# Kernel tuning notes

Hardware: AMD Instinct MI355X
Metric: run time of the kernel (lower is better)

Reference implementation:

```python
import jax, jax.numpy as jnp
import numpy as np

N_NODES = 100000
N_EDGES = 1600000
N_OBS = 48
HIDDEN = 48
N_ACT = 32


def setup_inputs() -> dict:
    key = jax.random.key(0)
    ks = jax.random.split(key, 6)
    x = jax.random.normal(ks[0], (N_OBS, N_NODES), dtype=jnp.float32)
    onehot = jax.random.uniform(ks[1], (1, N_NODES), dtype=jnp.float32)
    W1 = jax.random.normal(ks[2], (N_OBS, HIDDEN), dtype=jnp.float32) * (1.0 / np.sqrt(N_OBS))
    b1 = jnp.zeros((HIDDEN,), dtype=jnp.float32)
    W2 = jax.random.normal(ks[3], (HIDDEN, N_ACT), dtype=jnp.float32) * (1.0 / np.sqrt(HIDDEN))
    b2 = jnp.zeros((N_ACT,), dtype=jnp.float32)
    edge_index = jax.random.randint(ks[4], (2, N_EDGES), 0, N_NODES, dtype=jnp.int64)
    return {"x": x, "onehot": onehot, "W1": W1, "b1": b1, "W2": W2, "b2": b2, "edge_index": edge_index}


def reference(x, onehot, W1, b1, W2, b2, edge_index):
    # graph.x is stored transposed; forward does x = graph.x.T -> [N, F]
    h = x.T  # [N, n_obs]
    n = h.shape[0]
    # GCNConv default: add self-loops, symmetric deg^-1/2 normalization
    loops = jnp.arange(n, dtype=edge_index.dtype)
    row = jnp.concatenate([edge_index[0], loops])  # source nodes
    col = jnp.concatenate([edge_index[1], loops])  # target nodes
    deg = jax.ops.segment_sum(jnp.ones(row.shape, dtype=h.dtype), col, num_segments=n)
    dinv = jnp.where(deg > 0, jax.lax.rsqrt(jnp.maximum(deg, 1.0)), 0.0)
    norm = dinv[row] * dinv[col]  # [E+N]

    def conv(feat, W, b):
        feat = feat @ W                         # tiny dense GEMM [N, d_out]
        msg = norm[:, None] * feat[row]         # gather + scale  [E+N, d_out]
        return jax.ops.segment_sum(msg, col, num_segments=n) + b  # scatter-add

    # dropout is identity in eval mode
    h = jax.nn.relu(conv(h, W1, b1))
    h = conv(h, W2, b2)                          # [N, n_actions]
    return onehot @ h                            # [1, n_actions]
```

## Files before the change

kernel.cpp:

```cpp
#include <hip/hip_runtime.h>

#define CAP 64
#define NBUCK 512
#define NPB 196
#define NPH 98
#define GCAPH 1792
#define LCAP 24
#define GCAP 3584
#define NBIN 256
#define QAMAX0 6.0f
#define QS0 (127.0f / QAMAX0)
#define QAMAX1 4.0f
#define INVQS1 (QAMAX1 / 127.0f)
#define SMEM1 53248

__device__ __forceinline__ void bin_pass(const int* __restrict__ pay,
                                         const int* __restrict__ key, int E,
                                         int* __restrict__ bcur,
                                         unsigned* __restrict__ barr,
                                         char* smem, int binBlk) {
    unsigned* buf = (unsigned*)smem;
    int* cnt  = (int*)(buf + NBUCK * LCAP);
    int* base = cnt + NBUCK;
    for (int i = threadIdx.x; i < NBUCK; i += 256) cnt[i] = 0;
    __syncthreads();
    int epb = (E + NBIN - 1) / NBIN;
    int start = binBlk * epb;
    int end = min(E, start + epb);
    for (int e0 = start + threadIdx.x; e0 < end; e0 += 256 * 4) {
        int rr[4], cc[4];
#pragma unroll
        for (int k = 0; k < 4; k++) {
            int e = e0 + k * 256;
            if (e < end) { rr[k] = pay[e]; cc[k] = key[e]; }
        }
#pragma unroll
        for (int k = 0; k < 4; k++) {
            int e = e0 + k * 256;
            if (e < end) {
                int b = cc[k] / NPB;
                unsigned ent = ((unsigned)rr[k] << 8) | (unsigned)(cc[k] - b * NPB);
                int p = atomicAdd(&cnt[b], 1);
                if (p < LCAP) buf[b * LCAP + p] = ent;
                else {
                    int gp = atomicAdd(&bcur[b], 1);
                    if (gp < GCAP) barr[(size_t)b * GCAP + gp] = ent;
                }
            }
        }
    }
    __syncthreads();
    for (int b = threadIdx.x; b < NBUCK; b += 256)
        base[b] = atomicAdd(&bcur[b], min(cnt[b], LCAP));
    __syncthreads();
    for (int idx = threadIdx.x; idx < NBUCK * LCAP; idx += 256) {
        int b = idx / LCAP, slot = idx - b * LCAP;
        if (slot < min(cnt[b], LCAP)) {
            int gp = base[b] + slot;
            if (gp < GCAP) barr[(size_t)b * GCAP + gp] = buf[idx];
        }
    }
}

__launch_bounds__(256)
__global__ void k_bin_gemm(const int* __restrict__ row, const int* __restrict__ col,
                           int E, int* __restrict__ bcur1, unsigned* __restrict__ barr1,
                           int* __restrict__ bcur2, unsigned* __restrict__ barr2,
                           const float* __restrict__ x, const float* __restrict__ W1,
                           const float* __restrict__ onehot,
                           unsigned* __restrict__ q0, float* __restrict__ ohsum,
                           float* __restrict__ out, int N) {
    __shared__ __align__(16) char smem[SMEM1];
    if (blockIdx.x < NBIN) {
        bin_pass(row, col, E, bcur1, barr1, smem, blockIdx.x);
    } else if (blockIdx.x < 2 * NBIN) {
        bin_pass(col, row, E, bcur2, barr2, smem, blockIdx.x - NBIN);
    } else {
        if (blockIdx.x == 2 * NBIN && threadIdx.x < 32) out[threadIdx.x] = 0.f;
        float* Ws = (float*)smem;
        float* ohred = Ws + 48 * 48;
        for (int i = threadIdx.x; i < 48 * 48; i += 256) Ws[i] = W1[i];
        __syncthreads();
        int n = (blockIdx.x - 2 * NBIN) * 256 + threadIdx.x;
        float oh = 0.f;
        if (n < N) {
            float acc[48];
#pragma unroll
            for (int j = 0; j < 48; j++) acc[j] = 0.f;
            for (int k = 0; k < 48; k++) {
                float xv = x[(size_t)k * N + n];
#pragma unroll
                for (int j = 0; j < 48; j++) acc[j] += xv * Ws[k * 48 + j];
            }
            oh = onehot[n];
            unsigned* qp = q0 + (size_t)n * 12;
#pragma unroll
            for (int p = 0; p < 12; p++) {
                unsigned u = 0;
#pragma unroll
                for (int k = 0; k < 4; k++) {
                    int b = __float2int_rn(acc[4 * p + k] * QS0);
                    b = (b < -127 ? -127 : (b > 127 ? 127 : b)) + 128;
                    u |= ((unsigned)b) << (8 * k);
                }
                qp[p] = u;
            }
        }
        ohred[threadIdx.x] = oh;
        __syncthreads();
        for (int off = 128; off > 0; off >>= 1) {
            if (threadIdx.x < off) ohred[threadIdx.x] += ohred[threadIdx.x + off];
            __syncthreads();
        }
        if (threadIdx.x == 0) atomicAdd(ohsum, ohred[0]);
    }
}

__launch_bounds__(256)
__global__ void k_build(const unsigned* __restrict__ barr1,
                        const int* __restrict__ bcur1,
                        int* __restrict__ csr, long long* __restrict__ sd,
                        const float* __restrict__ onehot, float* __restrict__ t,
                        const unsigned* __restrict__ q0, unsigned* __restrict__ q,
                        int N) {
    __shared__ int csr_s[GCAPH];
    __shared__ int cnt_s[NPH];
    __shared__ int scan_s[128];
    __shared__ int cur_s[NPH];
    int b = blockIdx.x >> 1, half = blockIdx.x & 1;
    int lnbase = half * NPH;
    for (int i = threadIdx.x; i < NPH; i += 256) cnt_s[i] = 0;
    __syncthreads();
    int bn = min(bcur1[b], GCAP);
    const unsigned* bp = barr1 + (size_t)b * GCAP;
    int nbase = b * NPB + lnbase;
    for (int i = threadIdx.x; i < bn; i += 256) {
        int lnh = (int)(bp[i] & 0xffu) - lnbase;
        if ((unsigned)lnh < NPH) atomicAdd(&cnt_s[lnh], 1);
    }
    __syncthreads();
    int v = (threadIdx.x < NPH) ? cnt_s[threadIdx.x] : 0;
    if (threadIdx.x < 128) scan_s[threadIdx.x] = v;
    __syncthreads();
    for (int off = 1; off < 128; off <<= 1) {
        int tv = (threadIdx.x >= off && threadIdx.x < 128) ? scan_s[threadIdx.x - off] : 0;
        __syncthreads();
        if (threadIdx.x < 128) scan_s[threadIdx.x] += tv;
        __syncthreads();
    }
    if (threadIdx.x < NPH) cur_s[threadIdx.x] = scan_s[threadIdx.x] - v;
    __syncthreads();
    for (int i = threadIdx.x; i < bn; i += 256) {
        unsigned e = bp[i];
        int lnh = (int)(e & 0xffu) - lnbase;
        if ((unsigned)lnh < NPH) {
            int p = atomicAdd(&cur_s[lnh], 1);
            if (p < GCAPH) csr_s[p] = (int)(e >> 8);
        }
    }
    __syncthreads();
    int tot = min(scan_s[NPH - 1], GCAPH);
    int gbase = b * GCAP + half * GCAPH;
    for (int i = threadIdx.x; i < tot; i += 256)
        csr[gbase + i] = csr_s[i];
    for (int i = threadIdx.x; i < NPH; i += 256) {
        int n = nbase + i;
        if (n < N) {
            int d = cnt_s[i];
            long long st = (long long)(gbase + (scan_s[i] - d));
            sd[n] = st | ((long long)d << 32);
            t[n] = onehot[n] * rsqrtf((float)(d + 1));
        }
    }
    for (int idx = threadIdx.x; idx < NPH * 12; idx += 256) {
        int i = idx / 12, p = idx - i * 12;
        int n = nbase + i;
        if (n < N) {
            float r = 1.5f * rsqrtf((float)(cnt_s[i] + 1));
            unsigned u = q0[(size_t)n * 12 + p];
            unsigned o = 0;
#pragma unroll
            for (int k = 0; k < 4; k++) {
                int bq = (int)((u >> (8 * k)) & 0xffu) - 128;
                int nb = __float2int_rn((float)bq * r);
                nb = (nb < -127 ? -127 : (nb > 127 ? 127 : nb)) + 128;
                o |= ((unsigned)nb) << (8 * k);
            }
            q[(size_t)n * 12 + p] = o;
        }
    }
}

__launch_bounds__(256)
__global__ void k_gather_buildw(const unsigned* __restrict__ barr2,
                                const int* __restrict__ bcur2,
                                const float* __restrict__ t, float* __restrict__ w,
                                const int* __restrict__ csr,
                                const long long* __restrict__ sd,
                                const unsigned* __restrict__ q,
                                const float* __restrict__ b1, const float* __restrict__ W2,
                                float* __restrict__ g2, int N) {
    __shared__ float W2s[48 * 32];
    __shared__ float a1s[16][48];
    const unsigned M = 0x00FF00FFu;
    if (blockIdx.x < NBUCK) {
        float* wacc = (float*)W2s;
        int b = blockIdx.x;
        for (int i = threadIdx.x; i < NPB; i += 256) wacc[i] = 0.f;
        __syncthreads();
        int bn = min(bcur2[b], GCAP);
        const unsigned* bp = barr2 + (size_t)b * GCAP;
        int nbase = b * NPB;
        for (int i = threadIdx.x; i < bn; i += 256) {
            unsigned e = __builtin_nontemporal_load(&bp[i]);
            atomicAdd(&wacc[e & 0xffu], t[e >> 8]);
        }
        __syncthreads();
        for (int i = threadIdx.x; i < NPB; i += 256) {
            int n = nbase + i;
            if (n < N) w[n] = wacc[i] + t[n];
        }
        return;
    }
    for (int i = threadIdx.x; i < 48 * 32; i += 256) W2s[i] = W2[i];
    int wv = threadIdx.x >> 6, lane = threadIdx.x & 63;
    int quarter = lane >> 4, lane16 = lane & 15;
    int s = lane16 >> 2, j = lane16 & 3;
    int node = wv * 4 + quarter;
    int c = (blockIdx.x - NBUCK) * 16 + node;
    float dv = 0.f;
    if (c < N) {
        long long sdv = __builtin_nontemporal_load(&sd[c]);
        int beg = (int)(sdv & 0xffffffffLL), dg = (int)(sdv >> 32);
        int dd = dg < CAP ? dg : CAP;
        dv = rsqrtf((float)(dg + 1));
        int idx[4];
#pragma unroll
        for (int k = 0; k < 4; k++)
            idx[k] = (16 * k + lane16 < dd)
                         ? __builtin_nontemporal_load(&csr[beg + 16 * k + lane16]) : 0;
        unsigned ux[16], uy[16], uz[16];
#pragma unroll
        for (int g = 0; g < 16; g++) {
            if (4 * g < dd) {
                int e = 4 * g + s;
                int src = __shfl(idx[g >> 2], quarter * 16 + (e & 15));
                bool vld = (e < dd);
                const unsigned* qp = q + (size_t)src * 12 + 3 * j;
                ux[g] = vld ? qp[0] : 0u;
                uy[g] = vld ? qp[1] : 0u;
                uz[g] = vld ? qp[2] : 0u;
            }
        }
        unsigned aE0 = 0, aO0 = 0, aE1 = 0, aO1 = 0, aE2 = 0, aO2 = 0;
        if (s == 0) {
            const unsigned* qp = q + (size_t)c * 12 + 3 * j;
            unsigned x0 = qp[0], x1 = qp[1], x2 = qp[2];
            aE0 = x0 & M; aO0 = (x0 >> 8) & M;
            aE1 = x1 & M; aO1 = (x1 >> 8) & M;
            aE2 = x2 & M; aO2 = (x2 >> 8) & M;
        }
#pragma unroll
        for (int g = 0; g < 16; g++) {
            if (4 * g < dd) {
                aE0 += ux[g] & M; aO0 += (ux[g] >> 8) & M;
                aE1 += uy[g] & M; aO1 += (uy[g] >> 8) & M;
                aE2 += uz[g] & M; aO2 += (uz[g] >> 8) & M;
            }
        }
#pragma unroll
        for (int off = 8; off >= 4; off >>= 1) {
            aE0 += (unsigned)__shfl_down((int)aE0, off, 16);
            aO0 += (unsigned)__shfl_down((int)aO0, off, 16);
            aE1 += (unsigned)__shfl_down((int)aE1, off, 16);
            aO1 += (unsigned)__shfl_down((int)aO1, off, 16);
            aE2 += (unsigned)__shfl_down((int)aE2, off, 16);
            aO2 += (unsigned)__shfl_down((int)aO2, off, 16);
        }
        if (s == 0) {
            float cnt = (float)(dd + 1);
            float gsc = dv * INVQS1;
            float corr = 128.f * cnt;
            float S0 = (float)(aE0 & 0xffffu), S2 = (float)(aE0 >> 16);
            float S1 = (float)(aO0 & 0xffffu), S3 = (float)(aO0 >> 16);
            float S4 = (float)(aE1 & 0xffffu), S6 = (float)(aE1 >> 16);
            float S5 = (float)(aO1 & 0xffffu), S7 = (float)(aO1 >> 16);
            float S8 = (float)(aE2 & 0xffffu), S10 = (float)(aE2 >> 16);
            float S9 = (float)(aO2 & 0xffffu), S11 = (float)(aO2 >> 16);
            const float4* b4 = (const float4*)b1;
            float4 ba = b4[3 * j], bb = b4[3 * j + 1], bc = b4[3 * j + 2];
            float4 oa, ob, oc;
            oa.x = fmaxf(gsc * (S0 - corr) + ba.x, 0.f);
            oa.y = fmaxf(gsc * (S1 - corr) + ba.y, 0.f);
            oa.z = fmaxf(gsc * (S2 - corr) + ba.z, 0.f);
            oa.w = fmaxf(gsc * (S3 - corr) + ba.w, 0.f);
            ob.x = fmaxf(gsc * (S4 - corr) + bb.x, 0.f);
            ob.y = fmaxf(gsc * (S5 - corr) + bb.y, 0.f);
            ob.z = fmaxf(gsc * (S6 - corr) + bb.z, 0.f);
            ob.w = fmaxf(gsc * (S7 - corr) + bb.w, 0.f);
            oc.x = fmaxf(gsc * (S8 - corr) + bc.x, 0.f);
            oc.y = fmaxf(gsc * (S9 - corr) + bc.y, 0.f);
            oc.z = fmaxf(gsc * (S10 - corr) + bc.z, 0.f);
            oc.w = fmaxf(gsc * (S11 - corr) + bc.w, 0.f);
            float4* as4 = (float4*)a1s[node];
            as4[3 * j] = oa; as4[3 * j + 1] = ob; as4[3 * j + 2] = oc;
        }
    }
    __syncthreads();
    if (c < N) {
        int f0 = lane16 * 2;
        float a = 0.f, b = 0.f;
#pragma unroll
        for (int k = 0; k < 48; k++) {
            float av = a1s[node][k];
            a += av * W2s[k * 32 + f0];
            b += av * W2s[k * 32 + f0 + 1];
        }
        __builtin_nontemporal_store(dv * a, &g2[(size_t)c * 32 + f0]);
        __builtin_nontemporal_store(dv * b, &g2[(size_t)c * 32 + f0 + 1]);
    }
}

__global__ void k_final3(const float* __restrict__ g2, const float* __restrict__ w,
                         const float* __restrict__ ohsum, const float* __restrict__ b2,
                         float* __restrict__ out, int N) {
    __shared__ float s[256];
    int tid = threadIdx.x;
    int total = N * 32;
    int stride = gridDim.x * 256;
    float acc = 0.f;
    for (int i = blockIdx.x * 256 + tid; i < total; i += stride)
        acc += w[i >> 5] * g2[i];
    s[tid] = acc;
    __syncthreads();
    for (int off = 128; off >= 32; off >>= 1) {
        if (tid < off) s[tid] += s[tid + off];
        __syncthreads();
    }
    if (tid < 32) {
        float v = s[tid];
        if (blockIdx.x == 0) v += b2[tid] * ohsum[0];
        atomicAdd(&out[tid], v);
    }
}

extern "C" void kernel_launch(void* const* d_in, const int* in_sizes, int n_in,
                              void* d_out, int out_size, void* d_ws, size_t ws_size,
                              hipStream_t stream) {
    const float* x      = (const float*)d_in[0];
    const float* onehot = (const float*)d_in[1];
    const float* W1     = (const float*)d_in[2];
    const float* b1     = (const float*)d_in[3];
    const float* W2     = (const float*)d_in[4];
    const float* b2     = (const float*)d_in[5];
    const int*   ei     = (const int*)d_in[6];

    int N = in_sizes[1];
    int E = in_sizes[6] / 2;
    const int* row = ei;
    const int* col = ei + E;

    char* wsb = (char*)d_ws;
    int*       bcur1  = (int*)wsb;          wsb += 512 * 4;
    int*       bcur2  = (int*)wsb;          wsb += 512 * 4;
    float*     ohsum  = (float*)wsb;        wsb += 2 * 4;
    unsigned*  barr1  = (unsigned*)wsb;     wsb += (size_t)NBUCK * GCAP * 4;
    unsigned*  barr2  = (unsigned*)wsb;     wsb += (size_t)NBUCK * GCAP * 4;
    int*       csr    = (int*)wsb;          wsb += (size_t)NBUCK * GCAP * 4;
    long long* sd     = (long long*)wsb;    wsb += (size_t)N * 8;
    float*     t      = (float*)wsb;        wsb += (size_t)N * 4;
    float*     w      = (float*)wsb;        wsb += (size_t)N * 4;
    unsigned*  q0     = (unsigned*)wsb;     wsb += (size_t)N * 12 * 4;
    unsigned*  q      = (unsigned*)wsb;     wsb += (size_t)N * 12 * 4;
    float*     g2     = (float*)wsb;        wsb += (size_t)N * 32 * 4;

    hipMemsetAsync(bcur1, 0, (512 + 512 + 2) * 4, stream);

    int nGB = (N + 255) / 256;
    int NB = (N + 15) / 16;
    k_bin_gemm<<<2 * NBIN + nGB, 256, 0, stream>>>(row, col, E, bcur1, barr1,
                                                   bcur2, barr2, x, W1, onehot,
                                                   q0, ohsum, (float*)d_out, N);
    k_build<<<2 * NBUCK, 256, 0, stream>>>(barr1, bcur1, csr, sd,
                                           onehot, t, q0, q, N);
    k_gather_buildw<<<NBUCK + NB, 256, 0, stream>>>(barr2, bcur2, t, w,
                                                    csr, sd, q,
                                                    b1, W2, g2, N);
    k_final3<<<256, 256, 0, stream>>>(g2, w, ohsum, b2, (float*)d_out, N);
}
```

Baseline: 205.4 us.

## Replace CSR build with bucket-local shared-memory atomic aggregation of quantized features

```diff
diff --git a/kernel.cpp b/kernel.cpp
--- a/kernel.cpp
+++ b/kernel.cpp
@@ -1,10 +1,9 @@
 #include <hip/hip_runtime.h>
 
-#define CAP 64
 #define NBUCK 512
 #define NPB 196
 #define NPH 98
-#define GCAPH 1792
+#define ACCW 25
 #define LCAP 24
 #define GCAP 3584
 #define NBIN 256
@@ -117,62 +116,31 @@
 }
 
 __launch_bounds__(256)
-__global__ void k_build(const unsigned* __restrict__ barr1,
-                        const int* __restrict__ bcur1,
-                        int* __restrict__ csr, long long* __restrict__ sd,
-                        const float* __restrict__ onehot, float* __restrict__ t,
-                        const unsigned* __restrict__ q0, unsigned* __restrict__ q,
-                        int N) {
-    __shared__ int csr_s[GCAPH];
-    __shared__ int cnt_s[NPH];
-    __shared__ int scan_s[128];
-    __shared__ int cur_s[NPH];
-    int b = blockIdx.x >> 1, half = blockIdx.x & 1;
-    int lnbase = half * NPH;
-    for (int i = threadIdx.x; i < NPH; i += 256) cnt_s[i] = 0;
+__global__ void k_deg_rescale(const unsigned* __restrict__ barr1,
+                              const int* __restrict__ bcur1,
+                              const float* __restrict__ onehot,
+                              int* __restrict__ deg, float* __restrict__ t,
+                              const unsigned* __restrict__ q0,
+                              unsigned* __restrict__ q, int N) {
+    __shared__ int cnt_s[NPB];
+    int b = blockIdx.x;
+    for (int i = threadIdx.x; i < NPB; i += 256) cnt_s[i] = 0;
     __syncthreads();
     int bn = min(bcur1[b], GCAP);
     const unsigned* bp = barr1 + (size_t)b * GCAP;
-    int nbase = b * NPB + lnbase;
-    for (int i = threadIdx.x; i < bn; i += 256) {
-        int lnh = (int)(bp[i] & 0xffu) - lnbase;
-        if ((unsigned)lnh < NPH) atomicAdd(&cnt_s[lnh], 1);
-    }
-    __syncthreads();
-    int v = (threadIdx.x < NPH) ? cnt_s[threadIdx.x] : 0;
-    if (threadIdx.x < 128) scan_s[threadIdx.x] = v;
-    __syncthreads();
-    for (int off = 1; off < 128; off <<= 1) {
-        int tv = (threadIdx.x >= off && threadIdx.x < 128) ? scan_s[threadIdx.x - off] : 0;
-        __syncthreads();
-        if (threadIdx.x < 128) scan_s[threadIdx.x] += tv;
-        __syncthreads();
-    }
-    if (threadIdx.x < NPH) cur_s[threadIdx.x] = scan_s[threadIdx.x] - v;
-    __syncthreads();
-    for (int i = threadIdx.x; i < bn; i += 256) {
-        unsigned e = bp[i];
-        int lnh = (int)(e & 0xffu) - lnbase;
-        if ((unsigned)lnh < NPH) {
-            int p = atomicAdd(&cur_s[lnh], 1);
-            if (p < GCAPH) csr_s[p] = (int)(e >> 8);
-        }
-    }
-    __syncthreads();
-    int tot = min(scan_s[NPH - 1], GCAPH);
-    int gbase = b * GCAP + half * GCAPH;
-    for (int i = threadIdx.x; i < tot; i += 256)
-        csr[gbase + i] = csr_s[i];
-    for (int i = threadIdx.x; i < NPH; i += 256) {
+    for (int i = threadIdx.x; i < bn; i += 256)
+        atomicAdd(&cnt_s[bp[i] & 0xffu], 1);
+    __syncthreads();
+    int nbase = b * NPB;
+    for (int i = threadIdx.x; i < NPB; i += 256) {
         int n = nbase + i;
         if (n < N) {
             int d = cnt_s[i];
-            long long st = (long long)(gbase + (scan_s[i] - d));
-            sd[n] = st | ((long long)d << 32);
+            deg[n] = d;
             t[n] = onehot[n] * rsqrtf((float)(d + 1));
         }
     }
-    for (int idx = threadIdx.x; idx < NPH * 12; idx += 256) {
+    for (int idx = threadIdx.x; idx < NPB * 12; idx += 256) {
         int i = idx / 12, p = idx - i * 12;
         int n = nbase + i;
         if (n < N) {
@@ -186,138 +154,121 @@
                 nb = (nb < -127 ? -127 : (nb > 127 ? 127 : nb)) + 128;
                 o |= ((unsigned)nb) << (8 * k);
             }
-            q[(size_t)n * 12 + p] = o;
+            q[((size_t)n << 4) + p] = o;
         }
     }
 }
 
 __launch_bounds__(256)
-__global__ void k_gather_buildw(const unsigned* __restrict__ barr2,
+__global__ void k_gather_buildw(const unsigned* __restrict__ barr1,
+                                const int* __restrict__ bcur1,
+                                const unsigned* __restrict__ barr2,
                                 const int* __restrict__ bcur2,
+                                const int* __restrict__ deg,
                                 const float* __restrict__ t, float* __restrict__ w,
-                                const int* __restrict__ csr,
-                                const long long* __restrict__ sd,
                                 const unsigned* __restrict__ q,
-                                const float* __restrict__ b1, const float* __restrict__ W2,
+                                const float* __restrict__ b1,
+                                const float* __restrict__ W2,
                                 float* __restrict__ g2, int N) {
+    __shared__ unsigned acc_s[NPH][ACCW];
     __shared__ float W2s[48 * 32];
     __shared__ float a1s[16][48];
+    __shared__ float b1s[48];
+    __shared__ int deg_s[NPH];
     const unsigned M = 0x00FF00FFu;
-    if (blockIdx.x < NBUCK) {
+    int tid = threadIdx.x;
+    if (blockIdx.x >= 2 * NBUCK) {
         float* wacc = (float*)W2s;
-        int b = blockIdx.x;
-        for (int i = threadIdx.x; i < NPB; i += 256) wacc[i] = 0.f;
+        int b = blockIdx.x - 2 * NBUCK;
+        for (int i = tid; i < NPB; i += 256) wacc[i] = 0.f;
         __syncthreads();
         int bn = min(bcur2[b], GCAP);
         const unsigned* bp = barr2 + (size_t)b * GCAP;
         int nbase = b * NPB;
-        for (int i = threadIdx.x; i < bn; i += 256) {
+        for (int i = tid; i < bn; i += 256) {
             unsigned e = __builtin_nontemporal_load(&bp[i]);
             atomicAdd(&wacc[e & 0xffu], t[e >> 8]);
         }
         __syncthreads();
-        for (int i = threadIdx.x; i < NPB; i += 256) {
+        for (int i = tid; i < NPB; i += 256) {
             int n = nbase + i;
             if (n < N) w[n] = wacc[i] + t[n];
         }
         return;
     }
-    for (int i = threadIdx.x; i < 48 * 32; i += 256) W2s[i] = W2[i];
-    int wv = threadIdx.x >> 6, lane = threadIdx.x & 63;
-    int quarter = lane >> 4, lane16 = lane & 15;
-    int s = lane16 >> 2, j = lane16 & 3;
-    int node = wv * 4 + quarter;
-    int c = (blockIdx.x - NBUCK) * 16 + node;
-    float dv = 0.f;
-    if (c < N) {
-        long long sdv = __builtin_nontemporal_load(&sd[c]);
-        int beg = (int)(sdv & 0xffffffffLL), dg = (int)(sdv >> 32);
-        int dd = dg < CAP ? dg : CAP;
-        dv = rsqrtf((float)(dg + 1));
-        int idx[4];
-#pragma unroll
-        for (int k = 0; k < 4; k++)
-            idx[k] = (16 * k + lane16 < dd)
-                         ? __builtin_nontemporal_load(&csr[beg + 16 * k + lane16]) : 0;
-        unsigned ux[16], uy[16], uz[16];
-#pragma unroll
-        for (int g = 0; g < 16; g++) {
-            if (4 * g < dd) {
-                int e = 4 * g + s;
-                int src = __shfl(idx[g >> 2], quarter * 16 + (e & 15));
-                bool vld = (e < dd);
-                const unsigned* qp = q + (size_t)src * 12 + 3 * j;
-                ux[g] = vld ? qp[0] : 0u;
-                uy[g] = vld ? qp[1] : 0u;
-                uz[g] = vld ? qp[2] : 0u;
-            }
-        }
-        unsigned aE0 = 0, aO0 = 0, aE1 = 0, aO1 = 0, aE2 = 0, aO2 = 0;
-        if (s == 0) {
-            const unsigned* qp = q + (size_t)c * 12 + 3 * j;
-            unsigned x0 = qp[0], x1 = qp[1], x2 = qp[2];
-            aE0 = x0 & M; aO0 = (x0 >> 8) & M;
-            aE1 = x1 & M; aO1 = (x1 >> 8) & M;
-            aE2 = x2 & M; aO2 = (x2 >> 8) & M;
-        }
-#pragma unroll
-        for (int g = 0; g < 16; g++) {
-            if (4 * g < dd) {
-                aE0 += ux[g] & M; aO0 += (ux[g] >> 8) & M;
-                aE1 += uy[g] & M; aO1 += (uy[g] >> 8) & M;
-                aE2 += uz[g] & M; aO2 += (uz[g] >> 8) & M;
-            }
-        }
-#pragma unroll
-        for (int off = 8; off >= 4; off >>= 1) {
-            aE0 += (unsigned)__shfl_down((int)aE0, off, 16);
-            aO0 += (unsigned)__shfl_down((int)aO0, off, 16);
-            aE1 += (unsigned)__shfl_down((int)aE1, off, 16);
-            aO1 += (unsigned)__shfl_down((int)aO1, off, 16);
-            aE2 += (unsigned)__shfl_down((int)aE2, off, 16);
-            aO2 += (unsigned)__shfl_down((int)aO2, off, 16);
-        }
-        if (s == 0) {
-            float cnt = (float)(dd + 1);
+    int b = blockIdx.x >> 1, half = blockIdx.x & 1;
+    int lnbase = half * NPH;
+    int nbase = b * NPB + lnbase;
+    int grp = tid >> 2, j = tid & 3;
+    for (int i = tid; i < 48 * 32; i += 256) W2s[i] = W2[i];
+    if (tid < 48) b1s[tid] = b1[tid];
+    for (int i = tid; i < NPH; i += 256) {
+        int n = nbase + i;
+        deg_s[i] = (n < N) ? deg[n] : 0;
+    }
+    for (int i = grp; i < NPH; i += 64) {
+        if (j < 3) {
+            int n = nbase + i;
+            uint4 v = make_uint4(0u, 0u, 0u, 0u);
+            if (n < N) v = *(const uint4*)(q + ((size_t)n << 4) + 4 * j);
+            unsigned* a = acc_s[i] + 8 * j;
+            a[0] = v.x & M; a[1] = (v.x >> 8) & M;
+            a[2] = v.y & M; a[3] = (v.y >> 8) & M;
+            a[4] = v.z & M; a[5] = (v.z >> 8) & M;
+            a[6] = v.w & M; a[7] = (v.w >> 8) & M;
+        }
+    }
+    __syncthreads();
+    int bn = min(bcur1[b], GCAP);
+    const unsigned* bp = barr1 + (size_t)b * GCAP;
+#pragma unroll 2
+    for (int i = grp; i < bn; i += 64) {
+        unsigned e = bp[i];
+        int lnh = (int)(e & 0xffu) - lnbase;
+        if (j < 3 && (unsigned)lnh < NPH) {
+            uint4 v = *(const uint4*)(q + ((size_t)(e >> 8) << 4) + 4 * j);
+            unsigned* a = acc_s[lnh] + 8 * j;
+            atomicAdd(a + 0, v.x & M); atomicAdd(a + 1, (v.x >> 8) & M);
+            atomicAdd(a + 2, v.y & M); atomicAdd(a + 3, (v.y >> 8) & M);
+            atomicAdd(a + 4, v.z & M); atomicAdd(a + 5, (v.z >> 8) & M);
+            atomicAdd(a + 6, v.w & M); atomicAdd(a + 7, (v.w >> 8) & M);
+        }
+    }
+    __syncthreads();
+    int node16 = tid >> 4, lane16 = tid & 15;
+#pragma unroll
+    for (int c = 0; c < 7; c++) {
+        int i = c * 16 + node16;
+        int n = nbase + i;
+        bool valid = (i < NPH) && (n < N);
+        float dv = 0.f;
+        if (valid) {
+            float cnt = (float)(deg_s[i] + 1);
+            dv = rsqrtf(cnt);
             float gsc = dv * INVQS1;
             float corr = 128.f * cnt;
-            float S0 = (float)(aE0 & 0xffffu), S2 = (float)(aE0 >> 16);
-            float S1 = (float)(aO0 & 0xffffu), S3 = (float)(aO0 >> 16);
-            float S4 = (float)(aE1 & 0xffffu), S6 = (float)(aE1 >> 16);
-            float S5 = (float)(aO1 & 0xffffu), S7 = (float)(aO1 >> 16);
-            float S8 = (float)(aE2 & 0xffffu), S10 = (float)(aE2 >> 16);
-            float S9 = (float)(aO2 & 0xffffu), S11 = (float)(aO2 >> 16);
-            const float4* b4 = (const float4*)b1;
-            float4 ba = b4[3 * j], bb = b4[3 * j + 1], bc = b4[3 * j + 2];
-            float4 oa, ob, oc;
-            oa.x = fmaxf(gsc * (S0 - corr) + ba.x, 0.f);
-            oa.y = fmaxf(gsc * (S1 - corr) + ba.y, 0.f);
-            oa.z = fmaxf(gsc * (S2 - corr) + ba.z, 0.f);
-            oa.w = fmaxf(gsc * (S3 - corr) + ba.w, 0.f);
-            ob.x = fmaxf(gsc * (S4 - corr) + bb.x, 0.f);
-            ob.y = fmaxf(gsc * (S5 - corr) + bb.y, 0.f);
-            ob.z = fmaxf(gsc * (S6 - corr) + bb.z, 0.f);
-            ob.w = fmaxf(gsc * (S7 - corr) + bb.w, 0.f);
-            oc.x = fmaxf(gsc * (S8 - corr) + bc.x, 0.f);
-            oc.y = fmaxf(gsc * (S9 - corr) + bc.y, 0.f);
-            oc.z = fmaxf(gsc * (S10 - corr) + bc.z, 0.f);
-            oc.w = fmaxf(gsc * (S11 - corr) + bc.w, 0.f);
-            float4* as4 = (float4*)a1s[node];
-            as4[3 * j] = oa; as4[3 * j + 1] = ob; as4[3 * j + 2] = oc;
-        }
-    }
-    __syncthreads();
-    if (c < N) {
-        int f0 = lane16 * 2;
-        float a = 0.f, b = 0.f;
-#pragma unroll
-        for (int k = 0; k < 48; k++) {
-            float av = a1s[node][k];
-            a += av * W2s[k * 32 + f0];
-            b += av * W2s[k * 32 + f0 + 1];
-        }
-        __builtin_nontemporal_store(dv * a, &g2[(size_t)c * 32 + f0]);
-        __builtin_nontemporal_store(dv * b, &g2[(size_t)c * 32 + f0 + 1]);
+#pragma unroll
+            for (int ff = 0; ff < 3; ff++) {
+                int f = lane16 * 3 + ff;
+                unsigned av = acc_s[i][2 * (f >> 2) + (f & 1)];
+                float S = (float)((av >> (16 * ((f >> 1) & 1))) & 0xffffu);
+                a1s[node16][f] = fmaxf(gsc * (S - corr) + b1s[f], 0.f);
+            }
+        }
+        __syncthreads();
+        if (valid) {
+            int f0 = lane16 * 2;
+            float a = 0.f, bb = 0.f;
+#pragma unroll
+            for (int k = 0; k < 48; k++) {
+                float av = a1s[node16][k];
+                a += av * W2s[k * 32 + f0];
+                bb += av * W2s[k * 32 + f0 + 1];
+            }
+            __builtin_nontemporal_store(dv * a, &g2[(size_t)n * 32 + f0]);
+            __builtin_nontemporal_store(dv * bb, &g2[(size_t)n * 32 + f0 + 1]);
+        }
+        __syncthreads();
     }
 }
 
@@ -361,30 +312,26 @@
     const int* col = ei + E;
 
     char* wsb = (char*)d_ws;
-    int*       bcur1  = (int*)wsb;          wsb += 512 * 4;
-    int*       bcur2  = (int*)wsb;          wsb += 512 * 4;
-    float*     ohsum  = (float*)wsb;        wsb += 2 * 4;
+    int*       bcur1  = (int*)wsb;          wsb += NBUCK * 4;
+    int*       bcur2  = (int*)wsb;          wsb += NBUCK * 4;
+    float*     ohsum  = (float*)wsb;        wsb += 32;
     unsigned*  barr1  = (unsigned*)wsb;     wsb += (size_t)NBUCK * GCAP * 4;
     unsigned*  barr2  = (unsigned*)wsb;     wsb += (size_t)NBUCK * GCAP * 4;
-    int*       csr    = (int*)wsb;          wsb += (size_t)NBUCK * GCAP * 4;
-    long long* sd     = (long long*)wsb;    wsb += (size_t)N * 8;
+    int*       deg    = (int*)wsb;          wsb += (size_t)N * 4;
     float*     t      = (float*)wsb;        wsb += (size_t)N * 4;
     float*     w      = (float*)wsb;        wsb += (size_t)N * 4;
     unsigned*  q0     = (unsigned*)wsb;     wsb += (size_t)N * 12 * 4;
-    unsigned*  q      = (unsigned*)wsb;     wsb += (size_t)N * 12 * 4;
+    unsigned*  q      = (unsigned*)wsb;     wsb += (size_t)N * 16 * 4;
     float*     g2     = (float*)wsb;        wsb += (size_t)N * 32 * 4;
 
-    hipMemsetAsync(bcur1, 0, (512 + 512 + 2) * 4, stream);
+    hipMemsetAsync(bcur1, 0, NBUCK * 4 * 2 + 32, stream);
 
     int nGB = (N + 255) / 256;
-    int NB = (N + 15) / 16;
     k_bin_gemm<<<2 * NBIN + nGB, 256, 0, stream>>>(row, col, E, bcur1, barr1,
                                                    bcur2, barr2, x, W1, onehot,
                                                    q0, ohsum, (float*)d_out, N);
-    k_build<<<2 * NBUCK, 256, 0, stream>>>(barr1, bcur1, csr, sd,
-                                           onehot, t, q0, q, N);
-    k_gather_buildw<<<NBUCK + NB, 256, 0, stream>>>(barr2, bcur2, t, w,
-                                                    csr, sd, q,
-                                                    b1, W2, g2, N);
+    k_deg_rescale<<<NBUCK, 256, 0, stream>>>(barr1, bcur1, onehot, deg, t, q0, q, N);
+    k_gather_buildw<<<3 * NBUCK, 256, 0, stream>>>(barr1, bcur1, barr2, bcur2,
+                                                   deg, t, w, q, b1, W2, g2, N);
     k_final3<<<256, 256, 0, stream>>>(g2, w, ohsum, b2, (float*)d_out, N);
 }
```

Measured after the change: 208.4 us. About the same (+1.4%).
